# Performance work log

Hardware: AMD Instinct MI355X
Metric: run time of the kernel (lower is better)

The kernel has to match this reference:

```python
import jax, jax.numpy as jnp
import numpy as np

SEQ_LEN = 12
E = 64        # embedding_dim
H = 128       # h_dim
BNK = 1024    # bottleneck_dim
MLP = 1024    # mlp_dim
S, P = 32, 24 # scenes, peds per scene (uniform)
B = S * P


def setup_inputs() -> dict:
    key = jax.random.key(0)
    ks = jax.random.split(key, 24)
    w = lambda k, shape: jax.random.normal(k, shape, jnp.float32) * 0.05
    starts = jnp.arange(S, dtype=jnp.int32) * P
    return {
        'last_pos': jax.random.normal(ks[0], (B, 2), jnp.float32),
        'last_pos_rel': jax.random.normal(ks[1], (B, 2), jnp.float32),
        'h0': jax.random.normal(ks[2], (1, B, H), jnp.float32),
        'c0': jax.random.normal(ks[3], (1, B, H), jnp.float32),
        'seq_start_end': jnp.stack([starts, starts + P], axis=1),
        # decoder spatial embedding Linear(2, E)
        'W_se': w(ks[4], (2, E)), 'b_se': jnp.zeros((E,), jnp.float32),
        # LSTM (num_layers=1), PyTorch gate order i,f,g,o
        'W_ih': w(ks[5], (E, 4 * H)), 'b_ih': jnp.zeros((4 * H,), jnp.float32),
        'W_hh': w(ks[6], (H, 4 * H)), 'b_hh': jnp.zeros((4 * H,), jnp.float32),
        # hidden2pos Linear(H, 2)
        'W_hp': w(ks[7], (H, 2)), 'b_hp': jnp.zeros((2,), jnp.float32),
        # pool_net.spatial_embedding Linear(2, E)
        'W_pse': w(ks[8], (2, E)), 'b_pse': jnp.zeros((E,), jnp.float32),
        # pool_net.mlp_pre_pool [E+H, 512, BNK], ReLU, no batchnorm
        'W_p1': w(ks[9], (E + H, 512)), 'b_p1': jnp.zeros((512,), jnp.float32),
        'W_p2': w(ks[10], (512, BNK)), 'b_p2': jnp.zeros((BNK,), jnp.float32),
        # decoder.mlp [H+BNK, MLP, H], ReLU
        'W_m1': w(ks[11], (H + BNK, MLP)), 'b_m1': jnp.zeros((MLP,), jnp.float32),
        'W_m2': w(ks[12], (MLP, H)), 'b_m2': jnp.zeros((H,), jnp.float32),
    }


def reference(last_pos, last_pos_rel, h0, c0, seq_start_end,
              W_se, b_se, W_ih, b_ih, W_hh, b_hh, W_hp, b_hp,
              W_pse, b_pse, W_p1, b_p1, W_p2, b_p2, W_m1, b_m1, W_m2, b_m2):
    batch = last_pos.shape[0]
    n_scenes = seq_start_end.shape[0]
    peds = batch // n_scenes  # uniform scene sizes
    hdim = h0.shape[-1]

    dec_in0 = last_pos_rel @ W_se + b_se  # (B, E)

    def step(carry, _):
        lpos, dec_in, h, c = carry
        # single-step LSTM, PyTorch gate order i,f,g,o
        gates = dec_in @ W_ih + b_ih + h @ W_hh + b_hh  # (B, 4H)
        i, f, g, o = jnp.split(gates, 4, axis=-1)
        c_new = jax.nn.sigmoid(f) * c + jax.nn.sigmoid(i) * jnp.tanh(g)
        h_new = jax.nn.sigmoid(o) * jnp.tanh(c_new)
        rel_pos = h_new @ W_hp + b_hp            # (B, 2)
        curr_pos = rel_pos + lpos                # (B, 2)
        # --- PoolHiddenNet: pool_h[i] = max_j mlp([emb(pos_j - pos_i), h_j]) per scene ---
        pos = curr_pos.reshape(n_scenes, peds, 2)
        rel = pos[:, None, :, :] - pos[:, :, None, :]         # (S, Pi, Pj, 2), pos_j - pos_i
        emb = rel @ W_pse + b_pse                             # (S, Pi, Pj, E)
        hj = jnp.broadcast_to(h_new.reshape(n_scenes, 1, peds, hdim),
                              (n_scenes, peds, peds, hdim))   # h_j along axis 2
        x = jnp.concatenate([emb, hj], axis=-1)               # (S, Pi, Pj, E+H)
        x = jax.nn.relu(x @ W_p1 + b_p1)
        x = jax.nn.relu(x @ W_p2 + b_p2)                      # (S, Pi, Pj, BNK)
        pool_h = x.max(axis=2).reshape(batch, -1)             # (B, BNK)
        # --- decoder.mlp on [h, pool_h] -> new hidden state ---
        dh = jnp.concatenate([h_new, pool_h], axis=-1)
        dh = jax.nn.relu(dh @ W_m1 + b_m1)
        h_final = jax.nn.relu(dh @ W_m2 + b_m2)               # (B, H)
        dec_in_next = rel_pos @ W_se + b_se
        return (curr_pos, dec_in_next, h_final, c_new), rel_pos

    carry0 = (last_pos, dec_in0, h0[0], c0[0])
    (_, _, h_fin, _), pred_rel = jax.lax.scan(step, carry0, None, length=SEQ_LEN)
    return pred_rel, h_fin[None]  # (T, B, 2), (1, B, H)
```

## Files before the change

### kernel.cpp

```cpp
#include <hip/hip_runtime.h>
#include <math.h>

#define NB 768
#define NS 32
#define NP 24
#define ED 64
#define HD 128
#define G4 512
#define BNKD 1024
#define KM1 1152
#define TSTEPS 12
#define AR 4
#define BPITCH 516

typedef __bf16 bf16x8 __attribute__((ext_vector_type(8)));
typedef float f32x4 __attribute__((ext_vector_type(4)));
typedef unsigned short u16x8 __attribute__((ext_vector_type(8)));

__device__ __forceinline__ unsigned short f2bf(float f) {
  unsigned u = __float_as_uint(f);
  u = (u + 0x7FFFu + ((u >> 16) & 1u)) >> 16;
  return (unsigned short)u;
}
__device__ __forceinline__ unsigned pack2bf(float a, float b) {
  return (unsigned)f2bf(a) | ((unsigned)f2bf(b) << 16);
}
__device__ __forceinline__ float bf2f(unsigned short h) {
  return __uint_as_float(((unsigned)h) << 16);
}

__global__ void init_kernel(const float* __restrict__ last_pos,
                            const float* __restrict__ last_pos_rel,
                            const float* __restrict__ c0,
                            const float* __restrict__ W_se,
                            const float* __restrict__ b_se,
                            const float* __restrict__ W_pse,
                            const float* __restrict__ b_pse,
                            const float* __restrict__ W_p1,
                            const float* __restrict__ b_p1,
                            const float* __restrict__ W_p2,
                            const float* __restrict__ W_m1,
                            const float* __restrict__ W_m2,
                            float* __restrict__ ccar,
                            float* __restrict__ din, float* __restrict__ lpos,
                            float* __restrict__ Wc, float* __restrict__ bc,
                            unsigned short* __restrict__ W2T,
                            unsigned short* __restrict__ W1T,
                            unsigned short* __restrict__ WmT) {
  int stride = gridDim.x * blockDim.x;
  int idx0 = blockIdx.x * blockDim.x + threadIdx.x;
  for (int i = idx0; i < NB * HD; i += stride) ccar[i] = c0[i];
  for (int i = idx0; i < NB * 2; i += stride) lpos[i] = last_pos[i];
  for (int i = idx0; i < NB * ED; i += stride) {
    int r = i >> 6, e = i & 63;
    din[i] = b_se[e] + last_pos_rel[2 * r] * W_se[e]
                     + last_pos_rel[2 * r + 1] * W_se[ED + e];
  }
  for (int n = idx0; n < G4; n += stride) {
    float w0 = 0.f, w1 = 0.f, bb = b_p1[n];
    for (int e = 0; e < ED; ++e) {
      float wp = W_p1[e * G4 + n];
      w0 += W_pse[e] * wp;
      w1 += W_pse[ED + e] * wp;
      bb += b_pse[e] * wp;
    }
    Wc[n] = w0; Wc[G4 + n] = w1; bc[n] = bb;
  }
  for (int idx = idx0; idx < 1024 * 64; idx += stride) {
    int n = idx & 1023, k0 = (idx >> 10) << 3;
    unsigned pk0 = pack2bf(W_p2[(k0 + 0) * BNKD + n], W_p2[(k0 + 1) * BNKD + n]);
    unsigned pk1 = pack2bf(W_p2[(k0 + 2) * BNKD + n], W_p2[(k0 + 3) * BNKD + n]);
    unsigned pk2 = pack2bf(W_p2[(k0 + 4) * BNKD + n], W_p2[(k0 + 5) * BNKD + n]);
    unsigned pk3 = pack2bf(W_p2[(k0 + 6) * BNKD + n], W_p2[(k0 + 7) * BNKD + n]);
    *(uint4*)&W2T[n * G4 + k0] = make_uint4(pk0, pk1, pk2, pk3);
  }
  for (int idx = idx0; idx < 1024 * 144; idx += stride) {
    int n = idx & 1023, k0 = (idx >> 10) << 3;
    unsigned pk0 = pack2bf(W_m1[(k0 + 0) * BNKD + n], W_m1[(k0 + 1) * BNKD + n]);
    unsigned pk1 = pack2bf(W_m1[(k0 + 2) * BNKD + n], W_m1[(k0 + 3) * BNKD + n]);
    unsigned pk2 = pack2bf(W_m1[(k0 + 4) * BNKD + n], W_m1[(k0 + 5) * BNKD + n]);
    unsigned pk3 = pack2bf(W_m1[(k0 + 6) * BNKD + n], W_m1[(k0 + 7) * BNKD + n]);
    *(uint4*)&W1T[n * KM1 + k0] = make_uint4(pk0, pk1, pk2, pk3);
  }
  for (int idx = idx0; idx < 128 * 128; idx += stride) {
    int n = idx & 127, k0 = (idx >> 7) << 3;
    unsigned pk0 = pack2bf(W_m2[(k0 + 0) * HD + n], W_m2[(k0 + 1) * HD + n]);
    unsigned pk1 = pack2bf(W_m2[(k0 + 2) * HD + n], W_m2[(k0 + 3) * HD + n]);
    unsigned pk2 = pack2bf(W_m2[(k0 + 4) * HD + n], W_m2[(k0 + 5) * HD + n]);
    unsigned pk3 = pack2bf(W_m2[(k0 + 6) * HD + n], W_m2[(k0 + 7) * HD + n]);
    *(uint4*)&WmT[n * BNKD + k0] = make_uint4(pk0, pk1, pk2, pk3);
  }
}

__global__ __launch_bounds__(256) void step_a(
    const float* __restrict__ hprev, const float* __restrict__ cprev,
    const float* __restrict__ din, const float* __restrict__ lpos_in,
    const float* __restrict__ W_ih, const float* __restrict__ b_ih,
    const float* __restrict__ W_hh, const float* __restrict__ b_hh,
    const float* __restrict__ W_hp, const float* __restrict__ b_hp,
    const float* __restrict__ W_se, const float* __restrict__ b_se,
    const float* __restrict__ W_p1, const float* __restrict__ bc,
    const float* __restrict__ b_m2,
    float* __restrict__ hn, float* __restrict__ cnext,
    float* __restrict__ dnext, float* __restrict__ lpos_out,
    float* __restrict__ Hp1, float* __restrict__ pred_out,
    float* __restrict__ hacc_next, int relu_in) {
  __shared__ float x[AR][192];
  __shared__ float gg[AR][G4];
  __shared__ float hl[AR][HD];
  __shared__ float rp[AR][2];
  int t = threadIdx.x;
  int r0 = blockIdx.x * AR;

  for (int i = t; i < AR * ED; i += 256) { int r = i >> 6, k = i & 63; x[r][k] = din[(r0 + r) * ED + k]; }
  for (int i = t; i < AR * HD; i += 256) {
    int r = i >> 7, k = i & 127;
    float v = hprev[(r0 + r) * HD + k];
    if (relu_in) v = fmaxf(v, 0.f);
    x[r][ED + k] = v;
    hacc_next[(r0 + r) * HD + k] = b_m2[k];
  }
  __syncthreads();

  float acc[AR][2];
#pragma unroll
  for (int r = 0; r < AR; ++r) { acc[r][0] = b_ih[t] + b_hh[t]; acc[r][1] = b_ih[t + 256] + b_hh[t + 256]; }
  for (int k = 0; k < ED; ++k) {
    float w0 = W_ih[k * G4 + t], w1 = W_ih[k * G4 + t + 256];
#pragma unroll
    for (int r = 0; r < AR; ++r) { float a = x[r][k]; acc[r][0] += a * w0; acc[r][1] += a * w1; }
  }
  for (int k = 0; k < HD; ++k) {
    float w0 = W_hh[k * G4 + t], w1 = W_hh[k * G4 + t + 256];
#pragma unroll
    for (int r = 0; r < AR; ++r) { float a = x[r][ED + k]; acc[r][0] += a * w0; acc[r][1] += a * w1; }
  }
#pragma unroll
  for (int r = 0; r < AR; ++r) { gg[r][t] = acc[r][0]; gg[r][t + 256] = acc[r][1]; }
  __syncthreads();

  for (int i = t; i < AR * HD; i += 256) {
    int r = i >> 7, k = i & 127;
    float ig = gg[r][k], fg = gg[r][HD + k], gz = gg[r][2 * HD + k], og = gg[r][3 * HD + k];
    float si = 1.f / (1.f + expf(-ig));
    float sf = 1.f / (1.f + expf(-fg));
    float so = 1.f / (1.f + expf(-og));
    float gt = tanhf(gz);
    float c = sf * cprev[(r0 + r) * HD + k] + si * gt;
    float h = so * tanhf(c);
    cnext[(r0 + r) * HD + k] = c;
    hn[(r0 + r) * HD + k] = h;
    hl[r][k] = h;
  }
  __syncthreads();

  if (t < AR * 2) {
    int r = t >> 1, d = t & 1;
    float s = b_hp[d];
    for (int k = 0; k < HD; ++k) s += hl[r][k] * W_hp[k * 2 + d];
    rp[r][d] = s;
    pred_out[(r0 + r) * 2 + d] = s;
    lpos_out[(r0 + r) * 2 + d] = s + lpos_in[(r0 + r) * 2 + d];
  }
  __syncthreads();

  for (int i = t; i < AR * ED; i += 256) {
    int r = i >> 6, e = i & 63;
    dnext[(r0 + r) * ED + e] = b_se[e] + rp[r][0] * W_se[e] + rp[r][1] * W_se[ED + e];
  }

  float bc0 = bc[t], bc1 = bc[t + 256];
  float acc2[AR][2];
#pragma unroll
  for (int r = 0; r < AR; ++r) { acc2[r][0] = bc0; acc2[r][1] = bc1; }
  for (int k = 0; k < HD; ++k) {
    float w0 = W_p1[(ED + k) * G4 + t], w1 = W_p1[(ED + k) * G4 + t + 256];
#pragma unroll
    for (int r = 0; r < AR; ++r) { float a = hl[r][k]; acc2[r][0] += a * w0; acc2[r][1] += a * w1; }
  }
#pragma unroll
  for (int r = 0; r < AR; ++r) {
    Hp1[(r0 + r) * G4 + t] = acc2[r][0];
    Hp1[(r0 + r) * G4 + t + 256] = acc2[r][1];
  }
}

__global__ __launch_bounds__(256, 1) void pool_mfma(
    const float* __restrict__ curr_pos, const float* __restrict__ Hp1,
    const float* __restrict__ Wc,
    const unsigned short* __restrict__ W2T, const float* __restrict__ b_p2,
    float* __restrict__ pool_h) {
  __shared__ __align__(16) unsigned short Bl[128 * BPITCH];
  __shared__ __align__(16) unsigned short Hps[24 * BPITCH];
  __shared__ __align__(16) float wc0s[G4], wc1s[G4];
  __shared__ float psx[NP], psy[NP];
  int t = threadIdx.x;
  int b = blockIdx.x;
  int s = b >> 3, nt = b & 7;
  int n0 = nt * 128;

  for (int idx = t; idx < 128 * 64; idx += 256) {
    int row = idx >> 6, ch = (idx & 63) << 3;
    *(uint4*)&Bl[row * BPITCH + ch] = *(const uint4*)&W2T[(size_t)(n0 + row) * G4 + ch];
  }
  for (int idx = t; idx < 24 * 64; idx += 256) {
    int row = idx >> 6, ch = (idx & 63) << 3;
    const float* src = &Hp1[(size_t)(s * NP + row) * G4 + ch];
    float4 v0 = *(const float4*)src;
    float4 v1 = *(const float4*)(src + 4);
    uint4 pk;
    pk.x = pack2bf(v0.x, v0.y); pk.y = pack2bf(v0.z, v0.w);
    pk.z = pack2bf(v1.x, v1.y); pk.w = pack2bf(v1.z, v1.w);
    *(uint4*)&Hps[row * BPITCH + ch] = pk;
  }
  if (t < 128) {
    *(float4*)&wc0s[t * 4] = *(const float4*)&Wc[t * 4];
    *(float4*)&wc1s[t * 4] = *(const float4*)&Wc[G4 + t * 4];
  }
  if (t < NP) {
    psx[t] = curr_pos[(s * NP + t) * 2];
    psy[t] = curr_pos[(s * NP + t) * 2 + 1];
  }
  __syncthreads();

  int lane = t & 63, wv = t >> 6;
  int arow = lane & 15, ak = (lane >> 4) * 8;
  int h = lane >> 4;

  int boff[8];
#pragma unroll
  for (int nf = 0; nf < 8; ++nf) boff[nf] = (nf * 16 + arow) * BPITCH + ak;

  for (int c = 0; c < 3; ++c) {
    int ip = wv * 3 + c;
    float rx[3], ry[3];
    int hoff[3];
#pragma unroll
    for (int f = 0; f < 3; ++f) {
      int m = f * 16 + arow;
      int j = m % 24, g = m / 24;
      rx[f] = psx[j] - psx[ip * 2 + g];
      ry[f] = psy[j] - psy[ip * 2 + g];
      hoff[f] = j * BPITCH + ak;
    }
    f32x4 acc[3][8];
#pragma unroll
    for (int f = 0; f < 3; ++f)
#pragma unroll
      for (int nf = 0; nf < 8; ++nf) acc[f][nf] = (f32x4){0.f, 0.f, 0.f, 0.f};

#pragma unroll 2
    for (int kt = 0; kt < 16; ++kt) {
      int k0 = kt * 32;
      float4 wa = *(const float4*)&wc0s[k0 + ak];
      float4 wb = *(const float4*)&wc0s[k0 + ak + 4];
      float4 va = *(const float4*)&wc1s[k0 + ak];
      float4 vb = *(const float4*)&wc1s[k0 + ak + 4];
      bf16x8 af[3];
#pragma unroll
      for (int f = 0; f < 3; ++f) {
        u16x8 hp = *(const u16x8*)&Hps[hoff[f] + k0];
        float rxf = rx[f], ryf = ry[f];
        af[f][0] = (__bf16)fmaxf(bf2f(hp[0]) + rxf * wa.x + ryf * va.x, 0.f);
        af[f][1] = (__bf16)fmaxf(bf2f(hp[1]) + rxf * wa.y + ryf * va.y, 0.f);
        af[f][2] = (__bf16)fmaxf(bf2f(hp[2]) + rxf * wa.z + ryf * va.z, 0.f);
        af[f][3] = (__bf16)fmaxf(bf2f(hp[3]) + rxf * wa.w + ryf * va.w, 0.f);
        af[f][4] = (__bf16)fmaxf(bf2f(hp[4]) + rxf * wb.x + ryf * vb.x, 0.f);
        af[f][5] = (__bf16)fmaxf(bf2f(hp[5]) + rxf * wb.y + ryf * vb.y, 0.f);
        af[f][6] = (__bf16)fmaxf(bf2f(hp[6]) + rxf * wb.z + ryf * vb.z, 0.f);
        af[f][7] = (__bf16)fmaxf(bf2f(hp[7]) + rxf * wb.w + ryf * vb.w, 0.f);
      }
      bf16x8 bfr[8];
#pragma unroll
      for (int nf = 0; nf < 8; ++nf) bfr[nf] = *(const bf16x8*)&Bl[boff[nf] + k0];
#pragma unroll
      for (int nf = 0; nf < 8; ++nf)
#pragma unroll
        for (int f = 0; f < 3; ++f)
          acc[f][nf] = __builtin_amdgcn_mfma_f32_16x16x32_bf16(af[f], bfr[nf], acc[f][nf], 0, 0, 0);
    }

    int iA = s * NP + ip * 2;
#pragma unroll
    for (int nf = 0; nf < 8; ++nf) {
      f32x4 a0 = acc[0][nf], a1 = acc[1][nf], a2 = acc[2][nf];
      float v0 = fmaxf(fmaxf(a0[0], a0[1]), fmaxf(a0[2], a0[3]));
      float v1 = fmaxf(fmaxf(a1[0], a1[1]), fmaxf(a1[2], a1[3]));
      float v2 = fmaxf(fmaxf(a2[0], a2[1]), fmaxf(a2[2], a2[3]));
      v0 = fmaxf(v0, __shfl_xor(v0, 16));
      v1 = fmaxf(v1, __shfl_xor(v1, 16));
      v2 = fmaxf(v2, __shfl_xor(v2, 16));
      float xx = (h < 2) ? fmaxf(v0, v1) : v0;
      xx = fmaxf(xx, __shfl_xor(xx, 32));
      float yy = (h >= 2) ? fmaxf(v2, v1) : v2;
      yy = fmaxf(yy, __shfl_xor(yy, 32));
      int col = n0 + nf * 16 + (lane & 15);
      float bb = b_p2[col];
      xx = fmaxf(xx + bb, 0.f);
      yy = fmaxf(yy + bb, 0.f);
      if (h == 0) pool_h[(size_t)iA * BNKD + col] = xx;
      if (h == 1) pool_h[((size_t)iA + 1) * BNKD + col] = yy;
    }
  }
}

__global__ __launch_bounds__(256) void mlp1_fused(
    const float* __restrict__ hn, const float* __restrict__ ph,
    const unsigned short* __restrict__ W1T, const float* __restrict__ b_m1,
    const unsigned short* __restrict__ WmT, float* __restrict__ hacc) {
  __shared__ __align__(16) float Pl[32][132];
  int t = threadIdx.x, b = blockIdx.x;
  int mt = b >> 3, nt = b & 7;
  int r0 = mt * 32, n0 = nt * 128;
  int lane = t & 63, wid = t >> 6, wm = wid >> 1, wn = wid & 1;
  int arow = lane & 15, ak = (lane >> 4) * 8;
  int h = lane >> 4;

  f32x4 acc0[4];
#pragma unroll
  for (int nf = 0; nf < 4; ++nf) acc0[nf] = (f32x4){0.f, 0.f, 0.f, 0.f};
  int mrow = r0 + wm * 16 + arow;
  const unsigned short* bp[4];
#pragma unroll
  for (int nf = 0; nf < 4; ++nf)
    bp[nf] = W1T + (size_t)(n0 + wn * 64 + nf * 16 + arow) * KM1 + ak;
  const float* arow_h = hn + (size_t)mrow * HD;
  const float* arow_p = ph + (size_t)mrow * BNKD - HD;

  for (int kt = 0; kt < 36; ++kt) {
    int kg = kt * 32 + ak;
    const float* src = (kg < HD) ? arow_h : arow_p;
    float4 v0 = *(const float4*)&src[kg];
    float4 v1 = *(const float4*)&src[kg + 4];
    u16x8 ua;
    ua[0] = f2bf(v0.x); ua[1] = f2bf(v0.y); ua[2] = f2bf(v0.z); ua[3] = f2bf(v0.w);
    ua[4] = f2bf(v1.x); ua[5] = f2bf(v1.y); ua[6] = f2bf(v1.z); ua[7] = f2bf(v1.w);
    bf16x8 a = __builtin_bit_cast(bf16x8, ua);
#pragma unroll
    for (int nf = 0; nf < 4; ++nf) {
      bf16x8 bb = *(const bf16x8*)(bp[nf] + kt * 32);
      acc0[nf] = __builtin_amdgcn_mfma_f32_16x16x32_bf16(a, bb, acc0[nf], 0, 0, 0);
    }
  }

#pragma unroll
  for (int nf = 0; nf < 4; ++nf) {
    int colp = wn * 64 + nf * 16 + arow;
    float bb = b_m1[n0 + colp];
#pragma unroll
    for (int rr = 0; rr < 4; ++rr)
      Pl[wm * 16 + h * 4 + rr][colp] = fmaxf(acc0[nf][rr] + bb, 0.f);
  }
  __syncthreads();

  f32x4 acc2[4];
#pragma unroll
  for (int nf = 0; nf < 4; ++nf) acc2[nf] = (f32x4){0.f, 0.f, 0.f, 0.f};
  const unsigned short* b2p[4];
#pragma unroll
  for (int nf = 0; nf < 4; ++nf)
    b2p[nf] = WmT + (size_t)(wn * 64 + nf * 16 + arow) * BNKD + n0 + ak;
  const float* prow = &Pl[wm * 16 + arow][0];

#pragma unroll
  for (int k2 = 0; k2 < 4; ++k2) {
    u16x8 uh, ul;
#pragma unroll
    for (int q = 0; q < 8; ++q) {
      float vv = prow[k2 * 32 + ak + q];
      unsigned short hh = f2bf(vv);
      uh[q] = hh;
      ul[q] = f2bf(vv - bf2f(hh));
    }
    bf16x8 ahi = __builtin_bit_cast(bf16x8, uh);
    bf16x8 alo = __builtin_bit_cast(bf16x8, ul);
#pragma unroll
    for (int nf = 0; nf < 4; ++nf) {
      bf16x8 bb = *(const bf16x8*)(b2p[nf] + k2 * 32);
      acc2[nf] = __builtin_amdgcn_mfma_f32_16x16x32_bf16(ahi, bb, acc2[nf], 0, 0, 0);
      acc2[nf] = __builtin_amdgcn_mfma_f32_16x16x32_bf16(alo, bb, acc2[nf], 0, 0, 0);
    }
  }
#pragma unroll
  for (int nf = 0; nf < 4; ++nf)
#pragma unroll
    for (int rr = 0; rr < 4; ++rr)
      atomicAdd(&hacc[(size_t)(r0 + wm * 16 + h * 4 + rr) * HD + wn * 64 + nf * 16 + arow],
                acc2[nf][rr]);
}

__global__ void final_h(const float* __restrict__ hacc, float* __restrict__ out) {
  int i = blockIdx.x * 256 + threadIdx.x;
  if (i < NB * HD) out[i] = fmaxf(hacc[i], 0.f);
}

extern "C" void kernel_launch(void* const* d_in, const int* in_sizes, int n_in,
                              void* d_out, int out_size, void* d_ws, size_t ws_size,
                              hipStream_t stream) {
  const float* last_pos     = (const float*)d_in[0];
  const float* last_pos_rel = (const float*)d_in[1];
  const float* h0   = (const float*)d_in[2];
  const float* c0   = (const float*)d_in[3];
  const float* W_se = (const float*)d_in[5];
  const float* b_se = (const float*)d_in[6];
  const float* W_ih = (const float*)d_in[7];
  const float* b_ih = (const float*)d_in[8];
  const float* W_hh = (const float*)d_in[9];
  const float* b_hh = (const float*)d_in[10];
  const float* W_hp = (const float*)d_in[11];
  const float* b_hp = (const float*)d_in[12];
  const float* W_pse = (const float*)d_in[13];
  const float* b_pse = (const float*)d_in[14];
  const float* W_p1 = (const float*)d_in[15];
  const float* b_p1 = (const float*)d_in[16];
  const float* W_p2 = (const float*)d_in[17];
  const float* b_p2 = (const float*)d_in[18];
  const float* W_m1 = (const float*)d_in[19];
  const float* b_m1 = (const float*)d_in[20];
  const float* W_m2 = (const float*)d_in[21];
  const float* b_m2 = (const float*)d_in[22];

  float* ws = (float*)d_ws;
  float* hacc[2]  = { ws,           ws + 98304 };
  float* ccar[2]  = { ws + 196608,  ws + 294912 };
  float* din[2]   = { ws + 393216,  ws + 442368 };
  float* lposb[2] = { ws + 491520,  ws + 493056 };
  float* hn   = ws + 494592;
  float* Hp1  = ws + 592896;
  float* ph   = ws + 986112;
  float* Wc   = ws + 1772544;
  float* bc   = ws + 1773568;
  unsigned short* W2T = (unsigned short*)(ws + 1774080);
  unsigned short* W1T = (unsigned short*)(ws + 2036224);
  unsigned short* WmT = (unsigned short*)(ws + 2626048);

  float* pred = (float*)d_out;

  init_kernel<<<128, 256, 0, stream>>>(last_pos, last_pos_rel, c0,
                                       W_se, b_se, W_pse, b_pse, W_p1, b_p1,
                                       W_p2, W_m1, W_m2,
                                       ccar[0], din[0], lposb[0],
                                       Wc, bc, W2T, W1T, WmT);

  for (int t = 0; t < TSTEPS; ++t) {
    int a = t & 1, b = (t + 1) & 1;
    step_a<<<NB / AR, 256, 0, stream>>>(
        t == 0 ? h0 : hacc[a], ccar[a], din[a], lposb[a],
        W_ih, b_ih, W_hh, b_hh, W_hp, b_hp, W_se, b_se, W_p1, bc, b_m2,
        hn, ccar[b], din[b], lposb[b], Hp1, pred + t * NB * 2,
        hacc[b], t == 0 ? 0 : 1);
    pool_mfma<<<NS * 8, 256, 0, stream>>>(lposb[b], Hp1, Wc, W2T, b_p2, ph);
    mlp1_fused<<<192, 256, 0, stream>>>(hn, ph, W1T, b_m1, WmT, hacc[b]);
  }

  final_h<<<384, 256, 0, stream>>>(hacc[0], (float*)d_out + TSTEPS * NB * 2);
}
```

Baseline: 1.362 ms.

## Stage MLP input as packed bf16 buffer and widen pool kernel to 768 threads

The LSTM step and pool kernels now write h and pool_h straight into one packed bf16 row buffer (KM1 pitch), so mlp1 loads its A operand directly and no longer converts fp32 to bf16. LSTM and W_p1 weights are pre-converted to bf16 in init to halve weight traffic in step_a. The pool kernel moves from 256 threads looping over 3 ped pairs to 768 threads with one pair per wave, and the block index mapping is swapped so scenes vary fastest. Storing h in bf16 and converting weights to bf16 lowers precision, and the larger blocks change occupancy.

```diff
diff --git a/kernel.cpp b/kernel.cpp
--- a/kernel.cpp
+++ b/kernel.cpp
@@ -9,9 +9,11 @@
 #define G4 512
 #define BNKD 1024
 #define KM1 1152
+#define KG 192
 #define TSTEPS 12
 #define AR 4
 #define BPITCH 516
+#define HPITCH 516
 
 typedef __bf16 bf16x8 __attribute__((ext_vector_type(8)));
 typedef float f32x4 __attribute__((ext_vector_type(4)));
@@ -41,12 +43,16 @@
                             const float* __restrict__ W_p2,
                             const float* __restrict__ W_m1,
                             const float* __restrict__ W_m2,
+                            const float* __restrict__ W_ih,
+                            const float* __restrict__ W_hh,
                             float* __restrict__ ccar,
                             float* __restrict__ din, float* __restrict__ lpos,
                             float* __restrict__ Wc, float* __restrict__ bc,
                             unsigned short* __restrict__ W2T,
                             unsigned short* __restrict__ W1T,
-                            unsigned short* __restrict__ WmT) {
+                            unsigned short* __restrict__ WmT,
+                            unsigned short* __restrict__ Wgb,
+                            unsigned short* __restrict__ Wp1b) {
   int stride = gridDim.x * blockDim.x;
   int idx0 = blockIdx.x * blockDim.x + threadIdx.x;
   for (int i = idx0; i < NB * HD; i += stride) ccar[i] = c0[i];
@@ -90,18 +96,27 @@
     unsigned pk3 = pack2bf(W_m2[(k0 + 6) * HD + n], W_m2[(k0 + 7) * HD + n]);
     *(uint4*)&WmT[n * BNKD + k0] = make_uint4(pk0, pk1, pk2, pk3);
   }
+  for (int idx = idx0; idx < KG * G4; idx += stride) {
+    int k = idx >> 9, n = idx & 511;
+    float w = (k < ED) ? W_ih[k * G4 + n] : W_hh[(k - ED) * G4 + n];
+    Wgb[idx] = f2bf(w);
+  }
+  for (int idx = idx0; idx < HD * G4; idx += stride) {
+    int k = idx >> 9, n = idx & 511;
+    Wp1b[idx] = f2bf(W_p1[(ED + k) * G4 + n]);
+  }
 }
 
 __global__ __launch_bounds__(256) void step_a(
     const float* __restrict__ hprev, const float* __restrict__ cprev,
     const float* __restrict__ din, const float* __restrict__ lpos_in,
-    const float* __restrict__ W_ih, const float* __restrict__ b_ih,
-    const float* __restrict__ W_hh, const float* __restrict__ b_hh,
+    const unsigned short* __restrict__ Wgb,
+    const float* __restrict__ b_ih, const float* __restrict__ b_hh,
     const float* __restrict__ W_hp, const float* __restrict__ b_hp,
     const float* __restrict__ W_se, const float* __restrict__ b_se,
-    const float* __restrict__ W_p1, const float* __restrict__ bc,
+    const unsigned short* __restrict__ Wp1b, const float* __restrict__ bc,
     const float* __restrict__ b_m2,
-    float* __restrict__ hn, float* __restrict__ cnext,
+    unsigned short* __restrict__ mhA, float* __restrict__ cnext,
     float* __restrict__ dnext, float* __restrict__ lpos_out,
     float* __restrict__ Hp1, float* __restrict__ pred_out,
     float* __restrict__ hacc_next, int relu_in) {
@@ -125,15 +140,11 @@
   float acc[AR][2];
 #pragma unroll
   for (int r = 0; r < AR; ++r) { acc[r][0] = b_ih[t] + b_hh[t]; acc[r][1] = b_ih[t + 256] + b_hh[t + 256]; }
-  for (int k = 0; k < ED; ++k) {
-    float w0 = W_ih[k * G4 + t], w1 = W_ih[k * G4 + t + 256];
+#pragma unroll 4
+  for (int k = 0; k < KG; ++k) {
+    float w0 = bf2f(Wgb[k * G4 + t]), w1 = bf2f(Wgb[k * G4 + t + 256]);
 #pragma unroll
     for (int r = 0; r < AR; ++r) { float a = x[r][k]; acc[r][0] += a * w0; acc[r][1] += a * w1; }
-  }
-  for (int k = 0; k < HD; ++k) {
-    float w0 = W_hh[k * G4 + t], w1 = W_hh[k * G4 + t + 256];
-#pragma unroll
-    for (int r = 0; r < AR; ++r) { float a = x[r][ED + k]; acc[r][0] += a * w0; acc[r][1] += a * w1; }
   }
 #pragma unroll
   for (int r = 0; r < AR; ++r) { gg[r][t] = acc[r][0]; gg[r][t + 256] = acc[r][1]; }
@@ -149,7 +160,7 @@
     float c = sf * cprev[(r0 + r) * HD + k] + si * gt;
     float h = so * tanhf(c);
     cnext[(r0 + r) * HD + k] = c;
-    hn[(r0 + r) * HD + k] = h;
+    mhA[(size_t)(r0 + r) * KM1 + k] = f2bf(h);
     hl[r][k] = h;
   }
   __syncthreads();
@@ -173,8 +184,9 @@
   float acc2[AR][2];
 #pragma unroll
   for (int r = 0; r < AR; ++r) { acc2[r][0] = bc0; acc2[r][1] = bc1; }
+#pragma unroll 4
   for (int k = 0; k < HD; ++k) {
-    float w0 = W_p1[(ED + k) * G4 + t], w1 = W_p1[(ED + k) * G4 + t + 256];
+    float w0 = bf2f(Wp1b[k * G4 + t]), w1 = bf2f(Wp1b[k * G4 + t + 256]);
 #pragma unroll
     for (int r = 0; r < AR; ++r) { float a = hl[r][k]; acc2[r][0] += a * w0; acc2[r][1] += a * w1; }
   }
@@ -185,25 +197,25 @@
   }
 }
 
-__global__ __launch_bounds__(256, 1) void pool_mfma(
+__global__ __launch_bounds__(768, 1) void pool_fused(
     const float* __restrict__ curr_pos, const float* __restrict__ Hp1,
     const float* __restrict__ Wc,
     const unsigned short* __restrict__ W2T, const float* __restrict__ b_p2,
-    float* __restrict__ pool_h) {
+    unsigned short* __restrict__ mhA) {
   __shared__ __align__(16) unsigned short Bl[128 * BPITCH];
-  __shared__ __align__(16) unsigned short Hps[24 * BPITCH];
-  __shared__ __align__(16) float wc0s[G4], wc1s[G4];
+  __shared__ __align__(16) unsigned short Hs[24 * HPITCH];
+  __shared__ __align__(16) unsigned short wc0b[G4], wc1b[G4];
   __shared__ float psx[NP], psy[NP];
   int t = threadIdx.x;
   int b = blockIdx.x;
-  int s = b >> 3, nt = b & 7;
+  int s = b & 31, nt = b >> 5;
   int n0 = nt * 128;
 
-  for (int idx = t; idx < 128 * 64; idx += 256) {
+  for (int idx = t; idx < 128 * 64; idx += 768) {
     int row = idx >> 6, ch = (idx & 63) << 3;
     *(uint4*)&Bl[row * BPITCH + ch] = *(const uint4*)&W2T[(size_t)(n0 + row) * G4 + ch];
   }
-  for (int idx = t; idx < 24 * 64; idx += 256) {
+  for (int idx = t; idx < 24 * 64; idx += 768) {
     int row = idx >> 6, ch = (idx & 63) << 3;
     const float* src = &Hp1[(size_t)(s * NP + row) * G4 + ch];
     float4 v0 = *(const float4*)src;
@@ -211,11 +223,11 @@
     uint4 pk;
     pk.x = pack2bf(v0.x, v0.y); pk.y = pack2bf(v0.z, v0.w);
     pk.z = pack2bf(v1.x, v1.y); pk.w = pack2bf(v1.z, v1.w);
-    *(uint4*)&Hps[row * BPITCH + ch] = pk;
-  }
-  if (t < 128) {
-    *(float4*)&wc0s[t * 4] = *(const float4*)&Wc[t * 4];
-    *(float4*)&wc1s[t * 4] = *(const float4*)&Wc[G4 + t * 4];
+    *(uint4*)&Hs[row * HPITCH + ch] = pk;
+  }
+  for (int i = t; i < G4; i += 768) {
+    wc0b[i] = f2bf(Wc[i]);
+    wc1b[i] = f2bf(Wc[G4 + i]);
   }
   if (t < NP) {
     psx[t] = curr_pos[(s * NP + t) * 2];
@@ -224,88 +236,78 @@
   __syncthreads();
 
   int lane = t & 63, wv = t >> 6;
-  int arow = lane & 15, ak = (lane >> 4) * 8;
-  int h = lane >> 4;
-
+  int arow = lane & 15, ak = (lane >> 4) * 8, h = lane >> 4;
+  int ip = wv;
+
+  float rx[3], ry[3];
+  int hoff[3];
+#pragma unroll
+  for (int f = 0; f < 3; ++f) {
+    int m = f * 16 + arow;
+    int j = m % 24, g = m / 24;
+    rx[f] = psx[j] - psx[ip * 2 + g];
+    ry[f] = psy[j] - psy[ip * 2 + g];
+    hoff[f] = j * HPITCH + ak;
+  }
   int boff[8];
 #pragma unroll
   for (int nf = 0; nf < 8; ++nf) boff[nf] = (nf * 16 + arow) * BPITCH + ak;
 
-  for (int c = 0; c < 3; ++c) {
-    int ip = wv * 3 + c;
-    float rx[3], ry[3];
-    int hoff[3];
+  f32x4 acc[3][8];
+#pragma unroll
+  for (int f = 0; f < 3; ++f)
+#pragma unroll
+    for (int nf = 0; nf < 8; ++nf) acc[f][nf] = (f32x4){0.f, 0.f, 0.f, 0.f};
+
+  for (int kt = 0; kt < 16; ++kt) {
+    int k0 = kt * 32;
+    u16x8 w0v = *(const u16x8*)&wc0b[k0 + ak];
+    u16x8 w1v = *(const u16x8*)&wc1b[k0 + ak];
+    bf16x8 af[3];
 #pragma unroll
     for (int f = 0; f < 3; ++f) {
-      int m = f * 16 + arow;
-      int j = m % 24, g = m / 24;
-      rx[f] = psx[j] - psx[ip * 2 + g];
-      ry[f] = psy[j] - psy[ip * 2 + g];
-      hoff[f] = j * BPITCH + ak;
-    }
-    f32x4 acc[3][8];
-#pragma unroll
-    for (int f = 0; f < 3; ++f)
-#pragma unroll
-      for (int nf = 0; nf < 8; ++nf) acc[f][nf] = (f32x4){0.f, 0.f, 0.f, 0.f};
-
-#pragma unroll 2
-    for (int kt = 0; kt < 16; ++kt) {
-      int k0 = kt * 32;
-      float4 wa = *(const float4*)&wc0s[k0 + ak];
-      float4 wb = *(const float4*)&wc0s[k0 + ak + 4];
-      float4 va = *(const float4*)&wc1s[k0 + ak];
-      float4 vb = *(const float4*)&wc1s[k0 + ak + 4];
-      bf16x8 af[3];
-#pragma unroll
-      for (int f = 0; f < 3; ++f) {
-        u16x8 hp = *(const u16x8*)&Hps[hoff[f] + k0];
-        float rxf = rx[f], ryf = ry[f];
-        af[f][0] = (__bf16)fmaxf(bf2f(hp[0]) + rxf * wa.x + ryf * va.x, 0.f);
-        af[f][1] = (__bf16)fmaxf(bf2f(hp[1]) + rxf * wa.y + ryf * va.y, 0.f);
-        af[f][2] = (__bf16)fmaxf(bf2f(hp[2]) + rxf * wa.z + ryf * va.z, 0.f);
-        af[f][3] = (__bf16)fmaxf(bf2f(hp[3]) + rxf * wa.w + ryf * va.w, 0.f);
-        af[f][4] = (__bf16)fmaxf(bf2f(hp[4]) + rxf * wb.x + ryf * vb.x, 0.f);
-        af[f][5] = (__bf16)fmaxf(bf2f(hp[5]) + rxf * wb.y + ryf * vb.y, 0.f);
-        af[f][6] = (__bf16)fmaxf(bf2f(hp[6]) + rxf * wb.z + ryf * vb.z, 0.f);
-        af[f][7] = (__bf16)fmaxf(bf2f(hp[7]) + rxf * wb.w + ryf * vb.w, 0.f);
+      u16x8 hp = *(const u16x8*)&Hs[hoff[f] + k0];
+      float rxf = rx[f], ryf = ry[f];
+#pragma unroll
+      for (int q = 0; q < 8; ++q) {
+        float v = bf2f(hp[q]) + rxf * bf2f(w0v[q]) + ryf * bf2f(w1v[q]);
+        af[f][q] = (__bf16)fmaxf(v, 0.f);
       }
-      bf16x8 bfr[8];
-#pragma unroll
-      for (int nf = 0; nf < 8; ++nf) bfr[nf] = *(const bf16x8*)&Bl[boff[nf] + k0];
-#pragma unroll
-      for (int nf = 0; nf < 8; ++nf)
-#pragma unroll
-        for (int f = 0; f < 3; ++f)
-          acc[f][nf] = __builtin_amdgcn_mfma_f32_16x16x32_bf16(af[f], bfr[nf], acc[f][nf], 0, 0, 0);
-    }
-
-    int iA = s * NP + ip * 2;
+    }
 #pragma unroll
     for (int nf = 0; nf < 8; ++nf) {
-      f32x4 a0 = acc[0][nf], a1 = acc[1][nf], a2 = acc[2][nf];
-      float v0 = fmaxf(fmaxf(a0[0], a0[1]), fmaxf(a0[2], a0[3]));
-      float v1 = fmaxf(fmaxf(a1[0], a1[1]), fmaxf(a1[2], a1[3]));
-      float v2 = fmaxf(fmaxf(a2[0], a2[1]), fmaxf(a2[2], a2[3]));
-      v0 = fmaxf(v0, __shfl_xor(v0, 16));
-      v1 = fmaxf(v1, __shfl_xor(v1, 16));
-      v2 = fmaxf(v2, __shfl_xor(v2, 16));
-      float xx = (h < 2) ? fmaxf(v0, v1) : v0;
-      xx = fmaxf(xx, __shfl_xor(xx, 32));
-      float yy = (h >= 2) ? fmaxf(v2, v1) : v2;
-      yy = fmaxf(yy, __shfl_xor(yy, 32));
-      int col = n0 + nf * 16 + (lane & 15);
-      float bb = b_p2[col];
-      xx = fmaxf(xx + bb, 0.f);
-      yy = fmaxf(yy + bb, 0.f);
-      if (h == 0) pool_h[(size_t)iA * BNKD + col] = xx;
-      if (h == 1) pool_h[((size_t)iA + 1) * BNKD + col] = yy;
-    }
+      bf16x8 bfr = *(const bf16x8*)&Bl[boff[nf] + k0];
+      acc[0][nf] = __builtin_amdgcn_mfma_f32_16x16x32_bf16(af[0], bfr, acc[0][nf], 0, 0, 0);
+      acc[1][nf] = __builtin_amdgcn_mfma_f32_16x16x32_bf16(af[1], bfr, acc[1][nf], 0, 0, 0);
+      acc[2][nf] = __builtin_amdgcn_mfma_f32_16x16x32_bf16(af[2], bfr, acc[2][nf], 0, 0, 0);
+    }
+  }
+
+  int iA = s * NP + ip * 2;
+#pragma unroll
+  for (int nf = 0; nf < 8; ++nf) {
+    f32x4 a0 = acc[0][nf], a1 = acc[1][nf], a2 = acc[2][nf];
+    float v0 = fmaxf(fmaxf(a0[0], a0[1]), fmaxf(a0[2], a0[3]));
+    float v1 = fmaxf(fmaxf(a1[0], a1[1]), fmaxf(a1[2], a1[3]));
+    float v2 = fmaxf(fmaxf(a2[0], a2[1]), fmaxf(a2[2], a2[3]));
+    v0 = fmaxf(v0, __shfl_xor(v0, 16));
+    v1 = fmaxf(v1, __shfl_xor(v1, 16));
+    v2 = fmaxf(v2, __shfl_xor(v2, 16));
+    float xx = (h < 2) ? fmaxf(v0, v1) : v0;
+    xx = fmaxf(xx, __shfl_xor(xx, 32));
+    float yy = (h >= 2) ? fmaxf(v2, v1) : v2;
+    yy = fmaxf(yy, __shfl_xor(yy, 32));
+    int col = n0 + nf * 16 + (lane & 15);
+    float bb = b_p2[col];
+    xx = fmaxf(xx + bb, 0.f);
+    yy = fmaxf(yy + bb, 0.f);
+    if (h == 0) mhA[(size_t)iA * KM1 + HD + col] = f2bf(xx);
+    if (h == 1) mhA[((size_t)iA + 1) * KM1 + HD + col] = f2bf(yy);
   }
 }
 
 __global__ __launch_bounds__(256) void mlp1_fused(
-    const float* __restrict__ hn, const float* __restrict__ ph,
+    const unsigned short* __restrict__ mhA,
     const unsigned short* __restrict__ W1T, const float* __restrict__ b_m1,
     const unsigned short* __restrict__ WmT, float* __restrict__ hacc) {
   __shared__ __align__(16) float Pl[32][132];
@@ -324,18 +326,11 @@
 #pragma unroll
   for (int nf = 0; nf < 4; ++nf)
     bp[nf] = W1T + (size_t)(n0 + wn * 64 + nf * 16 + arow) * KM1 + ak;
-  const float* arow_h = hn + (size_t)mrow * HD;
-  const float* arow_p = ph + (size_t)mrow * BNKD - HD;
-
+  const unsigned short* arow_m = mhA + (size_t)mrow * KM1 + ak;
+
+#pragma unroll 4
   for (int kt = 0; kt < 36; ++kt) {
-    int kg = kt * 32 + ak;
-    const float* src = (kg < HD) ? arow_h : arow_p;
-    float4 v0 = *(const float4*)&src[kg];
-    float4 v1 = *(const float4*)&src[kg + 4];
-    u16x8 ua;
-    ua[0] = f2bf(v0.x); ua[1] = f2bf(v0.y); ua[2] = f2bf(v0.z); ua[3] = f2bf(v0.w);
-    ua[4] = f2bf(v1.x); ua[5] = f2bf(v1.y); ua[6] = f2bf(v1.z); ua[7] = f2bf(v1.w);
-    bf16x8 a = __builtin_bit_cast(bf16x8, ua);
+    bf16x8 a = *(const bf16x8*)(arow_m + kt * 32);
 #pragma unroll
     for (int nf = 0; nf < 4; ++nf) {
       bf16x8 bb = *(const bf16x8*)(bp[nf] + kt * 32);
@@ -425,32 +420,33 @@
   float* ccar[2]  = { ws + 196608,  ws + 294912 };
   float* din[2]   = { ws + 393216,  ws + 442368 };
   float* lposb[2] = { ws + 491520,  ws + 493056 };
-  float* hn   = ws + 494592;
-  float* Hp1  = ws + 592896;
-  float* ph   = ws + 986112;
-  float* Wc   = ws + 1772544;
-  float* bc   = ws + 1773568;
-  unsigned short* W2T = (unsigned short*)(ws + 1774080);
-  unsigned short* W1T = (unsigned short*)(ws + 2036224);
-  unsigned short* WmT = (unsigned short*)(ws + 2626048);
+  float* Hp1  = ws + 494592;
+  float* Wc   = ws + 887808;
+  float* bc   = ws + 888832;
+  unsigned short* W2T  = (unsigned short*)(ws + 889344);
+  unsigned short* W1T  = (unsigned short*)(ws + 1151488);
+  unsigned short* WmT  = (unsigned short*)(ws + 1741312);
+  unsigned short* mhA  = (unsigned short*)(ws + 1806848);
+  unsigned short* Wgb  = (unsigned short*)(ws + 2249216);
+  unsigned short* Wp1b = (unsigned short*)(ws + 2298368);
 
   float* pred = (float*)d_out;
 
   init_kernel<<<128, 256, 0, stream>>>(last_pos, last_pos_rel, c0,
                                        W_se, b_se, W_pse, b_pse, W_p1, b_p1,
-                                       W_p2, W_m1, W_m2,
+                                       W_p2, W_m1, W_m2, W_ih, W_hh,
                                        ccar[0], din[0], lposb[0],
-                                       Wc, bc, W2T, W1T, WmT);
+                                       Wc, bc, W2T, W1T, WmT, Wgb, Wp1b);
 
   for (int t = 0; t < TSTEPS; ++t) {
     int a = t & 1, b = (t + 1) & 1;
     step_a<<<NB / AR, 256, 0, stream>>>(
         t == 0 ? h0 : hacc[a], ccar[a], din[a], lposb[a],
-        W_ih, b_ih, W_hh, b_hh, W_hp, b_hp, W_se, b_se, W_p1, bc, b_m2,
-        hn, ccar[b], din[b], lposb[b], Hp1, pred + t * NB * 2,
+        Wgb, b_ih, b_hh, W_hp, b_hp, W_se, b_se, Wp1b, bc, b_m2,
+        mhA, ccar[b], din[b], lposb[b], Hp1, pred + t * NB * 2,
         hacc[b], t == 0 ? 0 : 1);
-    pool_mfma<<<NS * 8, 256, 0, stream>>>(lposb[b], Hp1, Wc, W2T, b_p2, ph);
-    mlp1_fused<<<192, 256, 0, stream>>>(hn, ph, W1T, b_m1, WmT, hacc[b]);
+    pool_fused<<<NS * 8, 768, 0, stream>>>(lposb[b], Hp1, Wc, W2T, b_p2, mhA);
+    mlp1_fused<<<192, 256, 0, stream>>>(mhA, W1T, b_m1, WmT, hacc[b]);
   }
 
   final_h<<<384, 256, 0, stream>>>(hacc[0], (float*)d_out + TSTEPS * NB * 2);
```

Result: faster. 1.167 ms (-14.3%).
